# Optimization experiments

Measured on AMD Instinct MI355X. Metric: run time of the kernel, lower is better.

## Reference

```python
import jax, jax.numpy as jnp
import numpy as np

# pywt haar dwt2 on even-sized input with any padding mode reduces to a 2x2
# orthonormal block transform (filter length 2, stride 2, no boundary effect):
#   cA (LL) = (x00 + x01 + x10 + x11)/2
#   cH (LH) = detail along rows (H axis), approx along cols: (x00 + x01 - x10 - x11)/2
#   cV (HL) = approx rows, detail cols: (x00 - x01 + x10 - x11)/2
#   cD (HH) = (x00 - x01 - x10 + x11)/2
# where x_ij = x[..., 2k+i, 2l+j]. Signs follow pywt dec_hi giving
# cD_1d[k] = (x[2k] - x[2k+1])/sqrt(2).

def _haar_dwt2(x):
    a00 = x[..., 0::2, 0::2]
    a01 = x[..., 0::2, 1::2]
    a10 = x[..., 1::2, 0::2]
    a11 = x[..., 1::2, 1::2]
    half = jnp.asarray(0.5, dtype=x.dtype)
    ll = (a00 + a01 + a10 + a11) * half
    lh = (a00 + a01 - a10 - a11) * half  # pywt cH
    hl = (a00 - a01 + a10 - a11) * half  # pywt cV
    hh = (a00 - a01 - a10 + a11) * half  # pywt cD
    return ll, lh, hl, hh


def setup_inputs() -> dict:
    key = jax.random.key(0)
    x = jax.random.normal(key, (8, 64, 512, 512), dtype=jnp.float32)
    return {"x": x}


def reference(x):
    return _haar_dwt2(x)
```

## Files before the change

### kernel.cpp

```cpp
#include <hip/hip_runtime.h>


__global__ __launch_bounds__(256) void dwt2_haar_kernel(
    const float* __restrict__ x, float* __restrict__ out, int total)
{
    const long long OUT_SZ = 512LL * 65536LL;

    float* __restrict__ oll = out;
    float* __restrict__ olh = out + OUT_SZ;
    float* __restrict__ ohl = out + 2 * OUT_SZ;
    float* __restrict__ ohh = out + 3 * OUT_SZ;

    for (int idx = blockIdx.x * blockDim.x + threadIdx.x; idx < total;
         idx += gridDim.x * blockDim.x) {
        int plane = idx >> 15;
        int rem   = idx & 32767;
        int i     = rem >> 7;
        int jp    = rem & 127;

        long long in_off = (long long)plane * 262144 + i * 1024 + jp * 4;
        float4 r0 = *reinterpret_cast<const float4*>(x + in_off);
        float4 r1 = *reinterpret_cast<const float4*>(x + in_off + 512);

        float2 ll, lh, hl, hh;
        {
            float a00 = r0.x, a01 = r0.y, a10 = r1.x, a11 = r1.y;
            ll.x = (a00 + a01 + a10 + a11) * 0.5f;
            lh.x = (a00 + a01 - a10 - a11) * 0.5f;
            hl.x = (a00 - a01 + a10 - a11) * 0.5f;
            hh.x = (a00 - a01 - a10 + a11) * 0.5f;
        }
        {
            float a00 = r0.z, a01 = r0.w, a10 = r1.z, a11 = r1.w;
            ll.y = (a00 + a01 + a10 + a11) * 0.5f;
            lh.y = (a00 + a01 - a10 - a11) * 0.5f;
            hl.y = (a00 - a01 + a10 - a11) * 0.5f;
            hh.y = (a00 - a01 - a10 + a11) * 0.5f;
        }

        long long o = (long long)plane * 65536 + i * 256 + jp * 2;
        *reinterpret_cast<float2*>(oll + o) = ll;
        *reinterpret_cast<float2*>(olh + o) = lh;
        *reinterpret_cast<float2*>(ohl + o) = hl;
        *reinterpret_cast<float2*>(ohh + o) = hh;
    }
}

extern "C" void kernel_launch(void* const* d_in, const int* in_sizes, int n_in,
                              void* d_out, int out_size, void* d_ws, size_t ws_size,
                              hipStream_t stream) {
    const float* x = (const float*)d_in[0];
    float* out = (float*)d_out;

    const int total = 512 * 256 * 128;
    const int block = 256;
    const int grid = 2048;

    dwt2_haar_kernel<<<grid, block, 0, stream>>>(x, out, total);
}
```

Measured before the change: 212.8 us.

## Pair lanes via shuffle to emit 16-byte stores with nontemporal wave-item loop

Reorganizes work into per-wave items where adjacent lanes exchange results with a 64-bit xor shuffle, so each lane writes one float4 to two of the four subbands instead of four float2 stores. Loads and stores use nontemporal builtins to avoid cache pollution for this streaming kernel, and the grid-stride loop is unrolled by two wave items. The aim is wider, fewer store instructions and more memory-level parallelism, at the cost of extra shuffles and selects.

```diff
diff --git a/kernel.cpp b/kernel.cpp
--- a/kernel.cpp
+++ b/kernel.cpp
@@ -1,8 +1,68 @@
 #include <hip/hip_runtime.h>
 
 
+typedef float v4f __attribute__((ext_vector_type(4)));
+typedef float v2f __attribute__((ext_vector_type(2)));
+
+__device__ __forceinline__ v2f shfl_xor1_f2(v2f v) {
+    union { v2f f; unsigned long long u; } c;
+    c.f = v;
+    c.u = __shfl_xor((unsigned long long)c.u, 1, 64);
+    return c.f;
+}
+
+__device__ __forceinline__ void dwt_wave_item(const float* __restrict__ x,
+                                              float* __restrict__ oll,
+                                              float* __restrict__ olh,
+                                              float* __restrict__ ohl,
+                                              float* __restrict__ ohh,
+                                              int wi, int lane)
+{
+    int plane = wi >> 9;
+    int rem   = wi & 511;
+    int i     = rem >> 1;
+    int h     = rem & 1;
+
+    long long in0 = (long long)plane * 262144 + (i << 10) + (h << 8) + (lane << 2);
+    v4f r0 = __builtin_nontemporal_load(reinterpret_cast<const v4f*>(x + in0));
+    v4f r1 = __builtin_nontemporal_load(reinterpret_cast<const v4f*>(x + in0 + 512));
+
+    v2f ll, lh, hl, hh;
+    {
+        float s0 = r0.x + r0.y, d0 = r0.x - r0.y;
+        float s1 = r1.x + r1.y, d1 = r1.x - r1.y;
+        ll.x = (s0 + s1) * 0.5f; lh.x = (s0 - s1) * 0.5f;
+        hl.x = (d0 + d1) * 0.5f; hh.x = (d0 - d1) * 0.5f;
+    }
+    {
+        float s0 = r0.z + r0.w, d0 = r0.z - r0.w;
+        float s1 = r1.z + r1.w, d1 = r1.z - r1.w;
+        ll.y = (s0 + s1) * 0.5f; lh.y = (s0 - s1) * 0.5f;
+        hl.y = (d0 + d1) * 0.5f; hh.y = (d0 - d1) * 0.5f;
+    }
+
+    v2f pll = shfl_xor1_f2(ll);
+    v2f plh = shfl_xor1_f2(lh);
+    v2f phl = shfl_xor1_f2(hl);
+    v2f phh = shfl_xor1_f2(hh);
+
+    bool odd = (lane & 1) != 0;
+    v4f s0v, s1v;
+    s0v.x = odd ? plh.x : ll.x;  s0v.y = odd ? plh.y : ll.y;
+    s0v.z = odd ? lh.x  : pll.x; s0v.w = odd ? lh.y  : pll.y;
+    s1v.x = odd ? phh.x : hl.x;  s1v.y = odd ? phh.y : hl.y;
+    s1v.z = odd ? hh.x  : phl.x; s1v.w = odd ? hh.y  : phl.y;
+
+    float* q0 = odd ? olh : oll;
+    float* q1 = odd ? ohh : ohl;
+
+    long long o = (long long)plane * 65536 + (i << 8) + (h << 7) + ((lane & ~1) << 1);
+    __builtin_nontemporal_store(s0v, reinterpret_cast<v4f*>(q0 + o));
+    __builtin_nontemporal_store(s1v, reinterpret_cast<v4f*>(q1 + o));
+}
+
 __global__ __launch_bounds__(256) void dwt2_haar_kernel(
-    const float* __restrict__ x, float* __restrict__ out, int total)
+    const float* __restrict__ x, float* __restrict__ out, int n_wave_items)
 {
     const long long OUT_SZ = 512LL * 65536LL;
 
@@ -11,38 +71,18 @@
     float* __restrict__ ohl = out + 2 * OUT_SZ;
     float* __restrict__ ohh = out + 3 * OUT_SZ;
 
-    for (int idx = blockIdx.x * blockDim.x + threadIdx.x; idx < total;
-         idx += gridDim.x * blockDim.x) {
-        int plane = idx >> 15;
-        int rem   = idx & 32767;
-        int i     = rem >> 7;
-        int jp    = rem & 127;
+    int tid  = blockIdx.x * blockDim.x + threadIdx.x;
+    int w    = tid >> 6;
+    int lane = tid & 63;
+    int nw   = (gridDim.x * blockDim.x) >> 6;
 
-        long long in_off = (long long)plane * 262144 + i * 1024 + jp * 4;
-        float4 r0 = *reinterpret_cast<const float4*>(x + in_off);
-        float4 r1 = *reinterpret_cast<const float4*>(x + in_off + 512);
-
-        float2 ll, lh, hl, hh;
-        {
-            float a00 = r0.x, a01 = r0.y, a10 = r1.x, a11 = r1.y;
-            ll.x = (a00 + a01 + a10 + a11) * 0.5f;
-            lh.x = (a00 + a01 - a10 - a11) * 0.5f;
-            hl.x = (a00 - a01 + a10 - a11) * 0.5f;
-            hh.x = (a00 - a01 - a10 + a11) * 0.5f;
-        }
-        {
-            float a00 = r0.z, a01 = r0.w, a10 = r1.z, a11 = r1.w;
-            ll.y = (a00 + a01 + a10 + a11) * 0.5f;
-            lh.y = (a00 + a01 - a10 - a11) * 0.5f;
-            hl.y = (a00 - a01 + a10 - a11) * 0.5f;
-            hh.y = (a00 - a01 - a10 + a11) * 0.5f;
-        }
-
-        long long o = (long long)plane * 65536 + i * 256 + jp * 2;
-        *reinterpret_cast<float2*>(oll + o) = ll;
-        *reinterpret_cast<float2*>(olh + o) = lh;
-        *reinterpret_cast<float2*>(ohl + o) = hl;
-        *reinterpret_cast<float2*>(ohh + o) = hh;
+    int wi = w;
+    for (; wi + nw < n_wave_items; wi += 2 * nw) {
+        dwt_wave_item(x, oll, olh, ohl, ohh, wi, lane);
+        dwt_wave_item(x, oll, olh, ohl, ohh, wi + nw, lane);
+    }
+    for (; wi < n_wave_items; wi += nw) {
+        dwt_wave_item(x, oll, olh, ohl, ohh, wi, lane);
     }
 }
 
@@ -52,9 +92,9 @@
     const float* x = (const float*)d_in[0];
     float* out = (float*)d_out;
 
-    const int total = 512 * 256 * 128;
+    const int n_wave_items = 512 * 256 * 2;
     const int block = 256;
     const int grid = 2048;
 
-    dwt2_haar_kernel<<<grid, block, 0, stream>>>(x, out, total);
+    dwt2_haar_kernel<<<grid, block, 0, stream>>>(x, out, n_wave_items);
 }
```

Measured after the change: 201.7 us. 5.2% less time.
